# Optimization experiments

Hardware: AMD Instinct MI355X
Metric: run time of the kernel (lower is better)

## Reference

```python
import jax, jax.numpy as jnp
import numpy as np

H = 4096          # hidden_size
NH = 32           # num query heads
NKV = 8           # num kv heads
HD = H // NH      # head_dim = 128
NE = 8            # num_experts
TOPK = 2
ROPE_THETA = 10000.0
EPS = 1e-6


def rmsnorm(x, w):
    var = jnp.mean(x * x, axis=-1, keepdims=True)
    return x * jax.lax.rsqrt(var + EPS) * w


def apply_rope_neox(x, positions):
    # x: [N, heads, HD]; neox style: rotate halves
    half = HD // 2
    inv_freq = 1.0 / (ROPE_THETA ** (jnp.arange(0, HD, 2, dtype=jnp.float32) / HD))  # [half]
    ang = positions.astype(jnp.float32)[:, None] * inv_freq[None, :]                 # [N, half]
    cos = jnp.cos(ang)[:, None, :]  # [N,1,half]
    sin = jnp.sin(ang)[:, None, :]
    x1, x2 = x[..., :half], x[..., half:]
    return jnp.concatenate([x1 * cos - x2 * sin, x2 * cos + x1 * sin], axis=-1)


def setup_inputs() -> dict:
    key = jax.random.key(0)
    ks = jax.random.split(key, 6)
    N = 2048
    return {
        "positions": jnp.arange(N, dtype=jnp.int32),
        "hidden_states": jax.random.normal(ks[0], (N, H), dtype=jnp.float32),
        "w_qkv": jax.random.normal(ks[1], (H, (NH + 2 * NKV) * HD), dtype=jnp.float32) * 0.02,
        "w_o": jax.random.normal(ks[2], (NH * HD, H), dtype=jnp.float32) * 0.02,
        "w_gate": jax.random.normal(ks[3], (H, NE), dtype=jnp.float32) * 0.02,
        "rms_w_pre": jnp.ones((H,), dtype=jnp.float32),
        "rms_w_post": jnp.ones((H,), dtype=jnp.float32),
        "expert_logits": jax.random.uniform(ks[4], (N, NE), dtype=jnp.float32),
    }


def reference(positions, hidden_states, w_qkv, w_o, w_gate, rms_w_pre, rms_w_post, expert_logits):
    N = hidden_states.shape[0]
    # pre-attention RMSNorm (residual is None branch)
    residual = hidden_states
    x = rmsnorm(hidden_states, rms_w_pre)

    qkv = x @ w_qkv
    q = qkv[:, : NH * HD].reshape(N, NH, HD)
    k = qkv[:, NH * HD : (NH + NKV) * HD].reshape(N, NKV, HD)
    v = qkv[:, (NH + NKV) * HD :].reshape(N, NKV, HD)

    q = apply_rope_neox(q, positions)
    k = apply_rope_neox(k, positions)

    # GQA causal self-attention (prefill, single sequence)
    group = NH // NKV
    k_rep = jnp.repeat(k, group, axis=1)  # [N, NH, HD]
    v_rep = jnp.repeat(v, group, axis=1)
    scale = HD ** -0.5
    scores = jnp.einsum("qhd,khd->hqk", q, k_rep) * scale  # [NH, N, N]
    causal = jnp.tril(jnp.ones((N, N), dtype=bool))
    scores = jnp.where(causal[None], scores, jnp.finfo(scores.dtype).min)
    probs = jax.nn.softmax(scores, axis=-1)
    attn_out = jnp.einsum("hqk,khd->qhd", probs, v_rep).reshape(N, NH * HD)

    output = attn_out @ w_o
    # post-attention RMSNorm with fused residual add (vLLM semantics)
    s = output + residual
    residual = s
    output = rmsnorm(s, rms_w_post)

    router_logits = output @ w_gate  # computed as in source; routing result overwritten below

    # random_routing: topk over random expert logits, renormalized
    topk_weights, topk_ids = jax.lax.top_k(expert_logits, TOPK)  # [N, TOPK]
    topk_weights = topk_weights / jnp.sum(topk_weights, axis=-1, keepdims=True)

    # permute_by_exp_ids: stable sort of flattened expert ids, gather tokens
    reorder_ids = jnp.argsort(topk_ids.reshape(-1), stable=True)  # [N*TOPK]
    permuted_output = output[reorder_ids // TOPK]                 # [N*TOPK, H]
    return permuted_output, topk_weights, topk_ids, reorder_ids
```

## Files before the change

kernel.cpp:

```cpp
#include <hip/hip_runtime.h>
#include <hip/hip_bf16.h>
#include <math.h>

#define N_TOK 2048
#define H_DIM 4096
#define NH 32
#define NKV 8
#define HD 128
#define QKV_D 6144
#define NE 8
#define TOPK 2

#define OUT_PERM 0
#define OUT_W    16777216
#define OUT_IDS  16781312
#define OUT_REO  16785408

typedef __bf16 bf16x8 __attribute__((ext_vector_type(8)));
typedef float f32x4 __attribute__((ext_vector_type(4)));

typedef __attribute__((address_space(3))) void lds_void;
typedef __attribute__((address_space(1))) const void gbl_void;

__device__ __forceinline__ void gld16(const void* g, void* l) {
    __builtin_amdgcn_global_load_lds((gbl_void*)g, (lds_void*)l, 16, 0, 0);
}

__device__ __forceinline__ unsigned short f2bf(float f) {
    union { float f; unsigned u; } v; v.f = f;
    unsigned r = v.u + 0x7fff + ((v.u >> 16) & 1);
    return (unsigned short)(r >> 16);
}
__device__ __forceinline__ unsigned pack2bf(float a, float b) {
    return (unsigned)f2bf(a) | ((unsigned)f2bf(b) << 16);
}
__device__ __forceinline__ float bf2f(unsigned short u) {
    union { unsigned u; float f; } v; v.u = ((unsigned)u) << 16;
    return v.f;
}

__global__ __launch_bounds__(256) void rmsnorm_k(const float* __restrict__ x,
                                                 const float* __restrict__ w,
                                                 float* __restrict__ yf,
                                                 unsigned short* __restrict__ yb) {
    int row = blockIdx.x;
    int tid = threadIdx.x;
    const float4* x4 = (const float4*)(x + (size_t)row * H_DIM);
    const float4* w4 = (const float4*)w;
    float4 v[4];
    float ss = 0.f;
#pragma unroll
    for (int k = 0; k < 4; ++k) {
        v[k] = x4[tid + k * 256];
        ss += v[k].x * v[k].x + v[k].y * v[k].y + v[k].z * v[k].z + v[k].w * v[k].w;
    }
#pragma unroll
    for (int off = 32; off; off >>= 1) ss += __shfl_xor(ss, off);
    __shared__ float sacc[4];
    if ((tid & 63) == 0) sacc[tid >> 6] = ss;
    __syncthreads();
    float tot = sacc[0] + sacc[1] + sacc[2] + sacc[3];
    float sc = rsqrtf(tot * (1.0f / H_DIM) + 1e-6f);
#pragma unroll
    for (int k = 0; k < 4; ++k) {
        float4 ww = w4[tid + k * 256];
        float4 o;
        o.x = v[k].x * sc * ww.x;
        o.y = v[k].y * sc * ww.y;
        o.z = v[k].z * sc * ww.z;
        o.w = v[k].w * sc * ww.w;
        if (yf) {
            *(float4*)(yf + (size_t)row * H_DIM + (tid + k * 256) * 4) = o;
        } else {
            uint2 p;
            p.x = pack2bf(o.x, o.y);
            p.y = pack2bf(o.z, o.w);
            *(uint2*)(yb + (size_t)row * H_DIM + (tid + k * 256) * 4) = p;
        }
    }
}

__global__ __launch_bounds__(256) void convT_k(const float* __restrict__ src,
                                               unsigned short* __restrict__ dst,
                                               int R, int C) {
    __shared__ float t[64][68];
    int r0 = blockIdx.y * 64, c0 = blockIdx.x * 64;
    int tid = threadIdx.x;
    int lr = tid >> 4, lc = tid & 15;
#pragma unroll
    for (int it = 0; it < 4; ++it) {
        int r = lr + it * 16;
        float4 v = *(const float4*)(src + (size_t)(r0 + r) * C + c0 + lc * 4);
        *(float4*)&t[r][lc * 4] = v;
    }
    __syncthreads();
#pragma unroll
    for (int it = 0; it < 4; ++it) {
        int cc = lr + it * 16;
        uint2 o;
        o.x = pack2bf(t[lc * 4 + 0][cc], t[lc * 4 + 1][cc]);
        o.y = pack2bf(t[lc * 4 + 2][cc], t[lc * 4 + 3][cc]);
        *(uint2*)(dst + (size_t)(c0 + cc) * R + r0 + lc * 4) = o;
    }
}

__global__ __launch_bounds__(256) void gemm_k(const __hip_bfloat16* __restrict__ A,
                                              const __hip_bfloat16* __restrict__ Bt,
                                              float* __restrict__ C,
                                              unsigned short* __restrict__ Cb,
                                              const float* __restrict__ residual,
                                              int Ncols) {
    __shared__ __align__(16) __hip_bfloat16 As[128 * 64];
    __shared__ __align__(16) __hip_bfloat16 Bs[128 * 64];
    const int K = H_DIM;
    int tid = threadIdx.x, w = tid >> 6, lane = tid & 63;
    int quad = lane >> 4, l15 = lane & 15;
    int m0 = blockIdx.x * 128, n0 = blockIdx.y * 128;
    int wm = (w & 1) * 64, wn = (w >> 1) * 64;

    int rowInChunk = lane >> 3;
    int uIdx = lane & 7;
    const char* Ag[4]; const char* Bg[4];
    char* Al[4]; char* Bl[4];
#pragma unroll
    for (int c = 0; c < 4; ++c) {
        int ch = w * 4 + c;
        int r = ch * 8 + rowInChunk;
        int gu = uIdx ^ (r & 7);
        Ag[c] = (const char*)(A + (size_t)(m0 + r) * K) + gu * 16;
        Bg[c] = (const char*)(Bt + (size_t)(n0 + r) * K) + gu * 16;
        Al[c] = (char*)As + ch * 1024;
        Bl[c] = (char*)Bs + ch * 1024;
    }

    f32x4 acc[4][4];
#pragma unroll
    for (int i = 0; i < 4; ++i)
#pragma unroll
        for (int j = 0; j < 4; ++j) acc[i][j] = (f32x4){0.f, 0.f, 0.f, 0.f};

    for (int k0 = 0; k0 < K; k0 += 64) {
        __syncthreads();
#pragma unroll
        for (int c = 0; c < 4; ++c) gld16(Ag[c] + (size_t)k0 * 2, Al[c]);
#pragma unroll
        for (int c = 0; c < 4; ++c) gld16(Bg[c] + (size_t)k0 * 2, Bl[c]);
        __syncthreads();
#pragma unroll
        for (int kk = 0; kk < 2; ++kk) {
            bf16x8 af[4], bfr[4];
#pragma unroll
            for (int mt = 0; mt < 4; ++mt) {
                int m = wm + mt * 16 + l15;
                af[mt] = *(const bf16x8*)((const char*)As + m * 128 + (((kk * 4 + quad) ^ (m & 7)) * 16));
            }
#pragma unroll
            for (int nt = 0; nt < 4; ++nt) {
                int n = wn + nt * 16 + l15;
                bfr[nt] = *(const bf16x8*)((const char*)Bs + n * 128 + (((kk * 4 + quad) ^ (n & 7)) * 16));
            }
#pragma unroll
            for (int mt = 0; mt < 4; ++mt)
#pragma unroll
                for (int nt = 0; nt < 4; ++nt)
                    acc[mt][nt] = __builtin_amdgcn_mfma_f32_16x16x32_bf16(af[mt], bfr[nt], acc[mt][nt], 0, 0, 0);
        }
    }
#pragma unroll
    for (int mt = 0; mt < 4; ++mt)
#pragma unroll
        for (int nt = 0; nt < 4; ++nt)
#pragma unroll
            for (int r = 0; r < 4; ++r) {
                int row = m0 + wm + mt * 16 + quad * 4 + r;
                int col = n0 + wn + nt * 16 + l15;
                size_t off = (size_t)row * Ncols + col;
                float v = acc[mt][nt][r];
                if (Cb) {
                    Cb[off] = f2bf(v);
                } else {
                    if (residual) v += residual[off];
                    C[off] = v;
                }
            }
}

__global__ __launch_bounds__(256) void prep_k(const unsigned short* __restrict__ qkvb,
                                              const int* __restrict__ pos,
                                              unsigned short* __restrict__ Qc,
                                              unsigned short* __restrict__ Kc) {
    int row = blockIdx.x, tid = threadIdx.x;
    float fpos = (float)pos[row];
    const float scale = 0.08838834764831845f;
    const float lg = 0.20762050593045f;
#pragma unroll
    for (int it = 0; it < 8; ++it) {
        int pi = tid + it * 256;
        int head = pi >> 6, t = pi & 63;
        float inv = exp2f(-(float)t * lg);
        float ang = fpos * inv;
        float s = __sinf(ang), c = __cosf(ang);
        const unsigned short* bp = qkvb + (size_t)row * QKV_D + head * HD + t;
        float x1 = bf2f(bp[0]), x2 = bf2f(bp[64]);
        unsigned short* qb = Qc + (size_t)row * H_DIM + head * HD + t;
        qb[0]  = f2bf((x1 * c - x2 * s) * scale);
        qb[64] = f2bf((x2 * c + x1 * s) * scale);
    }
#pragma unroll
    for (int it = 0; it < 2; ++it) {
        int pi = tid + it * 256;
        int kvh = pi >> 6, t = pi & 63;
        float inv = exp2f(-(float)t * lg);
        float ang = fpos * inv;
        float s = __sinf(ang), c = __cosf(ang);
        const unsigned short* bp = qkvb + (size_t)row * QKV_D + H_DIM + kvh * HD + t;
        float x1 = bf2f(bp[0]), x2 = bf2f(bp[64]);
        unsigned short* kb = Kc + ((size_t)kvh * N_TOK + row) * HD + t;
        kb[0]  = f2bf(x1 * c - x2 * s);
        kb[64] = f2bf(x2 * c + x1 * s);
    }
}

__global__ __launch_bounds__(256) void vt_k(const unsigned short* __restrict__ qkvb,
                                            unsigned short* __restrict__ Vt) {
    __shared__ unsigned short ts[64][136];
    int j0 = blockIdx.x * 64, kvh = blockIdx.y, tid = threadIdx.x;
#pragma unroll
    for (int it = 0; it < 4; ++it) {
        int idx = tid + it * 256;
        int r = idx >> 4, c8 = idx & 15;
        *(uint4*)&ts[r][c8 * 8] =
            *(const uint4*)(qkvb + (size_t)(j0 + r) * QKV_D + (NH + NKV) * HD + kvh * HD + c8 * 8);
    }
    __syncthreads();
    int d = tid >> 1, half = tid & 1;
    unsigned short* dst = Vt + ((size_t)kvh * HD + d) * N_TOK + j0 + half * 32;
#pragma unroll
    for (int g = 0; g < 4; ++g) {
        int kb = half * 32 + g * 8;
        uint4 o;
        o.x = (unsigned)ts[kb + 0][d] | ((unsigned)ts[kb + 1][d] << 16);
        o.y = (unsigned)ts[kb + 2][d] | ((unsigned)ts[kb + 3][d] << 16);
        o.z = (unsigned)ts[kb + 4][d] | ((unsigned)ts[kb + 5][d] << 16);
        o.w = (unsigned)ts[kb + 6][d] | ((unsigned)ts[kb + 7][d] << 16);
        *(uint4*)(dst + g * 8) = o;
    }
}

__global__ __launch_bounds__(256) void attn_k(const __hip_bfloat16* __restrict__ Qc,
                                              const __hip_bfloat16* __restrict__ Kc,
                                              const __hip_bfloat16* __restrict__ Vt,
                                              unsigned short* __restrict__ ao) {
    __shared__ __align__(16) __hip_bfloat16 Ks[32 * 128];
    __shared__ __align__(16) __hip_bfloat16 Vs[128 * 32];
    __shared__ __align__(16) unsigned short Pw[4][16 * 40];

    int tid = threadIdx.x, w = tid >> 6, lane = tid & 63;
    int quad = lane >> 4, l15 = lane & 15;
    int h = blockIdx.y, kvh = h >> 2;
    int qt = gridDim.x - 1 - blockIdx.x;
    int i0 = qt * 64;
    int i0q = i0 + w * 16;
    int q = i0q + l15;

    bf16x8 qf[4];
    const __hip_bfloat16* qrow = Qc + (size_t)q * H_DIM + h * HD;
#pragma unroll
    for (int kf = 0; kf < 4; ++kf)
        qf[kf] = *(const bf16x8*)(qrow + kf * 32 + quad * 8);

    const char* KcH = (const char*)(Kc + (size_t)kvh * N_TOK * HD);
    const char* VtH = (const char*)(Vt + (size_t)kvh * HD * N_TOK);

    int chA = w * 2, chB = chA + 1;
    int kKeyA = chA * 4 + (lane >> 4), kKeyB = chB * 4 + (lane >> 4);
    int kPartA = (lane & 15) ^ (kKeyA & 15), kPartB = (lane & 15) ^ (kKeyB & 15);
    int vDA = chA * 16 + (lane >> 2), vDB = chB * 16 + (lane >> 2);
    int vPA = (lane & 3) ^ (vDA & 3), vPB = (lane & 3) ^ (vDB & 3);
    char* KlA = (char*)Ks + chA * 1024;
    char* KlB = (char*)Ks + chB * 1024;
    char* VlA = (char*)Vs + chA * 1024;
    char* VlB = (char*)Vs + chB * 1024;

    float mstat = -INFINITY, lstat = 0.f;
    f32x4 o[8];
#pragma unroll
    for (int nt = 0; nt < 8; ++nt) o[nt] = (f32x4){0.f, 0.f, 0.f, 0.f};

    for (int j0 = 0; j0 < i0 + 64; j0 += 32) {
        __syncthreads();
        gld16(KcH + (size_t)(j0 + kKeyA) * 256 + kPartA * 16, KlA);
        gld16(KcH + (size_t)(j0 + kKeyB) * 256 + kPartB * 16, KlB);
        gld16(VtH + (size_t)vDA * (N_TOK * 2) + (size_t)j0 * 2 + vPA * 16, VlA);
        gld16(VtH + (size_t)vDB * (N_TOK * 2) + (size_t)j0 * 2 + vPB * 16, VlB);
        __syncthreads();
        if (j0 > i0q + 15) continue;

        f32x4 s[2];
        s[0] = (f32x4){0.f, 0.f, 0.f, 0.f};
        s[1] = (f32x4){0.f, 0.f, 0.f, 0.f};
#pragma unroll
        for (int mt = 0; mt < 2; ++mt) {
            int key = mt * 16 + l15;
#pragma unroll
            for (int kf = 0; kf < 4; ++kf) {
                bf16x8 kfr = *(const bf16x8*)((const char*)Ks + key * 256 + (((kf * 4 + quad) ^ (key & 15)) * 16));
                s[mt] = __builtin_amdgcn_mfma_f32_16x16x32_bf16(kfr, qf[kf], s[mt], 0, 0, 0);
            }
        }
        if (j0 + 31 > i0q) {
#pragma unroll
            for (int mt = 0; mt < 2; ++mt) {
                int keyb = j0 + mt * 16 + quad * 4;
#pragma unroll
                for (int r = 0; r < 4; ++r)
                    if (keyb + r > q) s[mt][r] = -INFINITY;
            }
        }
        float mx = fmaxf(fmaxf(fmaxf(s[0][0], s[0][1]), fmaxf(s[0][2], s[0][3])),
                         fmaxf(fmaxf(s[1][0], s[1][1]), fmaxf(s[1][2], s[1][3])));
        mx = fmaxf(mx, __shfl_xor(mx, 16));
        mx = fmaxf(mx, __shfl_xor(mx, 32));
        float newm = fmaxf(mstat, mx);
        float alpha = __expf(mstat - newm);
        float p[8];
#pragma unroll
        for (int mt = 0; mt < 2; ++mt)
#pragma unroll
            for (int r = 0; r < 4; ++r) p[mt * 4 + r] = __expf(s[mt][r] - newm);
        float ps = p[0] + p[1] + p[2] + p[3] + p[4] + p[5] + p[6] + p[7];
        ps += __shfl_xor(ps, 16);
        ps += __shfl_xor(ps, 32);
        lstat = lstat * alpha + ps;
        mstat = newm;

        unsigned* pwb = (unsigned*)(&Pw[w][0]);
        int eo = l15 * 20 + quad * 2;
        pwb[eo]     = pack2bf(p[0], p[1]);
        pwb[eo + 1] = pack2bf(p[2], p[3]);
        pwb[eo + 8] = pack2bf(p[4], p[5]);
        pwb[eo + 9] = pack2bf(p[6], p[7]);
        bf16x8 pf = *(const bf16x8*)(&Pw[w][l15 * 40 + quad * 8]);

        float alq[4];
#pragma unroll
        for (int r = 0; r < 4; ++r) alq[r] = __shfl(alpha, quad * 4 + r);
#pragma unroll
        for (int nt = 0; nt < 8; ++nt)
#pragma unroll
            for (int r = 0; r < 4; ++r) o[nt][r] *= alq[r];

#pragma unroll
        for (int nt = 0; nt < 8; ++nt) {
            int d = nt * 16 + l15;
            bf16x8 vf = *(const bf16x8*)((const char*)Vs + d * 64 + ((quad ^ (d & 3)) * 16));
            o[nt] = __builtin_amdgcn_mfma_f32_16x16x32_bf16(pf, vf, o[nt], 0, 0, 0);
        }
    }

    float linv[4];
#pragma unroll
    for (int r = 0; r < 4; ++r) linv[r] = 1.f / __shfl(lstat, quad * 4 + r);
#pragma unroll
    for (int nt = 0; nt < 8; ++nt)
#pragma unroll
        for (int r = 0; r < 4; ++r) {
            int row = i0q + quad * 4 + r;
            int col = h * HD + nt * 16 + l15;
            ao[(size_t)row * H_DIM + col] = f2bf(o[nt][r] * linv[r]);
        }
}

__global__ __launch_bounds__(256) void topk_k(const float* __restrict__ elog,
                                              float* __restrict__ w_out,
                                              float* __restrict__ id_out,
                                              int* __restrict__ ids_int) {
    int row = blockIdx.x * 256 + threadIdx.x;
    if (row >= N_TOK) return;
    const float4* e4 = (const float4*)(elog + (size_t)row * NE);
    float4 a = e4[0], b = e4[1];
    float e[8] = {a.x, a.y, a.z, a.w, b.x, b.y, b.z, b.w};
    int id0 = 0;
    float b0 = e[0];
#pragma unroll
    for (int t = 1; t < 8; ++t)
        if (e[t] > b0) { b0 = e[t]; id0 = t; }
    int id1 = -1;
    float b1 = -INFINITY;
#pragma unroll
    for (int t = 0; t < 8; ++t)
        if (t != id0 && e[t] > b1) { b1 = e[t]; id1 = t; }
    float s = b0 + b1;
    w_out[row * 2 + 0] = b0 / s;
    w_out[row * 2 + 1] = b1 / s;
    id_out[row * 2 + 0] = (float)id0;
    id_out[row * 2 + 1] = (float)id1;
    ids_int[row * 2 + 0] = id0;
    ids_int[row * 2 + 1] = id1;
}

__global__ __launch_bounds__(256) void sort_k(const int* __restrict__ ids,
                                              float* __restrict__ reorder_out,
                                              int* __restrict__ perm) {
    __shared__ int sh[N_TOK * TOPK];
    int tid = threadIdx.x;
    for (int r = tid; r < N_TOK * TOPK; r += 256) sh[r] = ids[r];
    __syncthreads();
    int i = blockIdx.x * 256 + tid;
    int e = sh[i];
    int rank = 0;
    for (int j = 0; j < N_TOK * TOPK; ++j) {
        int ej = sh[j];
        rank += (ej < e) ? 1 : ((ej == e && j < i) ? 1 : 0);
    }
    reorder_out[rank] = (float)i;
    perm[rank] = i;
}

__global__ __launch_bounds__(256) void gather_k(const float* __restrict__ src,
                                                const int* __restrict__ perm,
                                                float* __restrict__ dst) {
    int r = blockIdx.x;
    int srow = perm[r] >> 1;
    const float4* s4 = (const float4*)(src + (size_t)srow * H_DIM);
    float4* d4 = (float4*)(dst + (size_t)r * H_DIM);
    int tid = threadIdx.x;
#pragma unroll
    for (int k = 0; k < 4; ++k) d4[tid + k * 256] = s4[tid + k * 256];
}

extern "C" void kernel_launch(void* const* d_in, const int* in_sizes, int n_in,
                              void* d_out, int out_size, void* d_ws, size_t ws_size,
                              hipStream_t stream) {
    const int*   positions = (const int*)d_in[0];
    const float* hidden    = (const float*)d_in[1];
    const float* w_qkv     = (const float*)d_in[2];
    const float* w_o       = (const float*)d_in[3];
    const float* rms_pre   = (const float*)d_in[5];
    const float* rms_post  = (const float*)d_in[6];
    const float* elog      = (const float*)d_in[7];
    float* out = (float*)d_out;

    char* ws = (char*)d_ws;
    unsigned short* wqkvT = (unsigned short*)(ws);
    unsigned short* woT   = (unsigned short*)(ws);
    float*          post  = (float*)(ws + 33554432ULL);
    unsigned short* xn    = (unsigned short*)(ws + 50331648ULL);
    unsigned short* aout  = (unsigned short*)(ws + 50331648ULL);
    unsigned short* qkvb  = (unsigned short*)(ws + 67108864ULL);
    float*          sbuf  = (float*)(ws + 67108864ULL);
    unsigned short* Qc    = (unsigned short*)(ws + 117440512ULL);
    unsigned short* Kc    = (unsigned short*)(ws + 134217728ULL);
    unsigned short* Vt    = (unsigned short*)(ws + 138412032ULL);
    int* ids_int  = (int*)(ws + 142606336ULL);
    int* perm_int = (int*)(ws + 142622720ULL);

    convT_k<<<dim3(QKV_D / 64, H_DIM / 64), 256, 0, stream>>>(w_qkv, wqkvT, H_DIM, QKV_D);
    rmsnorm_k<<<N_TOK, 256, 0, stream>>>(hidden, rms_pre, nullptr, xn);
    gemm_k<<<dim3(N_TOK / 128, QKV_D / 128), 256, 0, stream>>>(
        (const __hip_bfloat16*)xn, (const __hip_bfloat16*)wqkvT, nullptr, qkvb, nullptr, QKV_D);
    convT_k<<<dim3(H_DIM / 64, H_DIM / 64), 256, 0, stream>>>(w_o, woT, H_DIM, H_DIM);
    prep_k<<<N_TOK, 256, 0, stream>>>(qkvb, positions, Qc, Kc);
    vt_k<<<dim3(N_TOK / 64, NKV), 256, 0, stream>>>(qkvb, Vt);
    attn_k<<<dim3(N_TOK / 64, NH), 256, 0, stream>>>(
        (const __hip_bfloat16*)Qc, (const __hip_bfloat16*)Kc, (const __hip_bfloat16*)Vt, aout);
    gemm_k<<<dim3(N_TOK / 128, H_DIM / 128), 256, 0, stream>>>(
        (const __hip_bfloat16*)aout, (const __hip_bfloat16*)woT, sbuf, nullptr, hidden, H_DIM);
    rmsnorm_k<<<N_TOK, 256, 0, stream>>>(sbuf, rms_post, post, nullptr);
    topk_k<<<N_TOK / 256, 256, 0, stream>>>(elog, out + OUT_W, out + OUT_IDS, ids_int);
    sort_k<<<(N_TOK * TOPK) / 256, 256, 0, stream>>>(ids_int, out + OUT_REO, perm_int);
    gather_k<<<N_TOK * TOPK, 256, 0, stream>>>(post, perm_int, out + OUT_PERM);
}
```

Before: 799.9 us.

## Share KV tiles across two GQA heads per block and double-buffer K/V loads

The attention kernel now runs 512-thread blocks in which the 8 waves cover two query heads that share one KV head, so each K/V tile loaded into LDS serves twice as many heads. K/V tiles are double-buffered: the next tile is prefetched with async global-to-LDS loads while the current one is computed, which cuts the per-step barriers from two to one. The aim is to reduce K/V global traffic and hide load latency. The cost is doubled LDS for K/V, larger blocks that may lower occupancy, and half as many blocks in the grid.

```diff
diff --git a/kernel.cpp b/kernel.cpp
--- a/kernel.cpp
+++ b/kernel.cpp
@@ -247,20 +247,22 @@
     }
 }
 
-__global__ __launch_bounds__(256) void attn_k(const __hip_bfloat16* __restrict__ Qc,
+__global__ __launch_bounds__(512) void attn_k(const __hip_bfloat16* __restrict__ Qc,
                                               const __hip_bfloat16* __restrict__ Kc,
                                               const __hip_bfloat16* __restrict__ Vt,
                                               unsigned short* __restrict__ ao) {
-    __shared__ __align__(16) __hip_bfloat16 Ks[32 * 128];
-    __shared__ __align__(16) __hip_bfloat16 Vs[128 * 32];
-    __shared__ __align__(16) unsigned short Pw[4][16 * 40];
+    __shared__ __align__(16) __hip_bfloat16 Ks[2][32 * 128];
+    __shared__ __align__(16) __hip_bfloat16 Vs[2][128 * 32];
+    __shared__ __align__(16) unsigned short Pw[8][16 * 40];
 
     int tid = threadIdx.x, w = tid >> 6, lane = tid & 63;
     int quad = lane >> 4, l15 = lane & 15;
-    int h = blockIdx.y, kvh = h >> 2;
+    int pr = blockIdx.y;
+    int kvh = pr >> 1;
+    int h = kvh * 4 + (pr & 1) * 2 + (w & 1);
     int qt = gridDim.x - 1 - blockIdx.x;
     int i0 = qt * 64;
-    int i0q = i0 + w * 16;
+    int i0q = i0 + (w >> 1) * 16;
     int q = i0q + l15;
 
     bf16x8 qf[4];
@@ -272,90 +274,98 @@
     const char* KcH = (const char*)(Kc + (size_t)kvh * N_TOK * HD);
     const char* VtH = (const char*)(Vt + (size_t)kvh * HD * N_TOK);
 
-    int chA = w * 2, chB = chA + 1;
-    int kKeyA = chA * 4 + (lane >> 4), kKeyB = chB * 4 + (lane >> 4);
-    int kPartA = (lane & 15) ^ (kKeyA & 15), kPartB = (lane & 15) ^ (kKeyB & 15);
-    int vDA = chA * 16 + (lane >> 2), vDB = chB * 16 + (lane >> 2);
-    int vPA = (lane & 3) ^ (vDA & 3), vPB = (lane & 3) ^ (vDB & 3);
-    char* KlA = (char*)Ks + chA * 1024;
-    char* KlB = (char*)Ks + chB * 1024;
-    char* VlA = (char*)Vs + chA * 1024;
-    char* VlB = (char*)Vs + chB * 1024;
+    int kKey = w * 4 + (lane >> 4);
+    int kPart = (lane & 15) ^ (kKey & 15);
+    int vD = w * 16 + (lane >> 2);
+    int vP = (lane & 3) ^ (vD & 3);
+    char* Kl[2] = { (char*)&Ks[0][0] + w * 1024, (char*)&Ks[1][0] + w * 1024 };
+    char* Vl[2] = { (char*)&Vs[0][0] + w * 1024, (char*)&Vs[1][0] + w * 1024 };
 
     float mstat = -INFINITY, lstat = 0.f;
     f32x4 o[8];
 #pragma unroll
     for (int nt = 0; nt < 8; ++nt) o[nt] = (f32x4){0.f, 0.f, 0.f, 0.f};
 
-    for (int j0 = 0; j0 < i0 + 64; j0 += 32) {
+    int nsteps = (i0 + 64) >> 5;
+
+    gld16(KcH + (size_t)kKey * 256 + kPart * 16, Kl[0]);
+    gld16(VtH + (size_t)vD * (N_TOK * 2) + vP * 16, Vl[0]);
+    __syncthreads();
+
+    for (int t = 0; t < nsteps; ++t) {
+        int j0 = t << 5;
+        int cur = t & 1;
+        if (t + 1 < nsteps) {
+            int jn = j0 + 32;
+            gld16(KcH + (size_t)(jn + kKey) * 256 + kPart * 16, Kl[cur ^ 1]);
+            gld16(VtH + (size_t)vD * (N_TOK * 2) + (size_t)jn * 2 + vP * 16, Vl[cur ^ 1]);
+        }
+        if (j0 <= i0q + 15) {
+            const char* Kb = (const char*)&Ks[cur][0];
+            const char* Vb = (const char*)&Vs[cur][0];
+
+            f32x4 s[2];
+            s[0] = (f32x4){0.f, 0.f, 0.f, 0.f};
+            s[1] = (f32x4){0.f, 0.f, 0.f, 0.f};
+#pragma unroll
+            for (int mt = 0; mt < 2; ++mt) {
+                int key = mt * 16 + l15;
+#pragma unroll
+                for (int kf = 0; kf < 4; ++kf) {
+                    bf16x8 kfr = *(const bf16x8*)(Kb + key * 256 + (((kf * 4 + quad) ^ (key & 15)) * 16));
+                    s[mt] = __builtin_amdgcn_mfma_f32_16x16x32_bf16(kfr, qf[kf], s[mt], 0, 0, 0);
+                }
+            }
+            if (j0 + 31 > i0q) {
+#pragma unroll
+                for (int mt = 0; mt < 2; ++mt) {
+                    int keyb = j0 + mt * 16 + quad * 4;
+#pragma unroll
+                    for (int r = 0; r < 4; ++r)
+                        if (keyb + r > q) s[mt][r] = -INFINITY;
+                }
+            }
+            float mx = fmaxf(fmaxf(fmaxf(s[0][0], s[0][1]), fmaxf(s[0][2], s[0][3])),
+                             fmaxf(fmaxf(s[1][0], s[1][1]), fmaxf(s[1][2], s[1][3])));
+            mx = fmaxf(mx, __shfl_xor(mx, 16));
+            mx = fmaxf(mx, __shfl_xor(mx, 32));
+            float newm = fmaxf(mstat, mx);
+            float alpha = __expf(mstat - newm);
+            float p[8];
+#pragma unroll
+            for (int mt = 0; mt < 2; ++mt)
+#pragma unroll
+                for (int r = 0; r < 4; ++r) p[mt * 4 + r] = __expf(s[mt][r] - newm);
+            float ps = p[0] + p[1] + p[2] + p[3] + p[4] + p[5] + p[6] + p[7];
+            ps += __shfl_xor(ps, 16);
+            ps += __shfl_xor(ps, 32);
+            lstat = lstat * alpha + ps;
+            mstat = newm;
+
+            unsigned* pwb = (unsigned*)(&Pw[w][0]);
+            int eo = l15 * 20 + quad * 2;
+            pwb[eo]     = pack2bf(p[0], p[1]);
+            pwb[eo + 1] = pack2bf(p[2], p[3]);
+            pwb[eo + 8] = pack2bf(p[4], p[5]);
+            pwb[eo + 9] = pack2bf(p[6], p[7]);
+            bf16x8 pf = *(const bf16x8*)(&Pw[w][l15 * 40 + quad * 8]);
+
+            float alq[4];
+#pragma unroll
+            for (int r = 0; r < 4; ++r) alq[r] = __shfl(alpha, quad * 4 + r);
+#pragma unroll
+            for (int nt = 0; nt < 8; ++nt)
+#pragma unroll
+                for (int r = 0; r < 4; ++r) o[nt][r] *= alq[r];
+
+#pragma unroll
+            for (int nt = 0; nt < 8; ++nt) {
+                int d = nt * 16 + l15;
+                bf16x8 vf = *(const bf16x8*)(Vb + d * 64 + ((quad ^ (d & 3)) * 16));
+                o[nt] = __builtin_amdgcn_mfma_f32_16x16x32_bf16(pf, vf, o[nt], 0, 0, 0);
+            }
+        }
         __syncthreads();
-        gld16(KcH + (size_t)(j0 + kKeyA) * 256 + kPartA * 16, KlA);
-        gld16(KcH + (size_t)(j0 + kKeyB) * 256 + kPartB * 16, KlB);
-        gld16(VtH + (size_t)vDA * (N_TOK * 2) + (size_t)j0 * 2 + vPA * 16, VlA);
-        gld16(VtH + (size_t)vDB * (N_TOK * 2) + (size_t)j0 * 2 + vPB * 16, VlB);
-        __syncthreads();
-        if (j0 > i0q + 15) continue;
-
-        f32x4 s[2];
-        s[0] = (f32x4){0.f, 0.f, 0.f, 0.f};
-        s[1] = (f32x4){0.f, 0.f, 0.f, 0.f};
-#pragma unroll
-        for (int mt = 0; mt < 2; ++mt) {
-            int key = mt * 16 + l15;
-#pragma unroll
-            for (int kf = 0; kf < 4; ++kf) {
-                bf16x8 kfr = *(const bf16x8*)((const char*)Ks + key * 256 + (((kf * 4 + quad) ^ (key & 15)) * 16));
-                s[mt] = __builtin_amdgcn_mfma_f32_16x16x32_bf16(kfr, qf[kf], s[mt], 0, 0, 0);
-            }
-        }
-        if (j0 + 31 > i0q) {
-#pragma unroll
-            for (int mt = 0; mt < 2; ++mt) {
-                int keyb = j0 + mt * 16 + quad * 4;
-#pragma unroll
-                for (int r = 0; r < 4; ++r)
-                    if (keyb + r > q) s[mt][r] = -INFINITY;
-            }
-        }
-        float mx = fmaxf(fmaxf(fmaxf(s[0][0], s[0][1]), fmaxf(s[0][2], s[0][3])),
-                         fmaxf(fmaxf(s[1][0], s[1][1]), fmaxf(s[1][2], s[1][3])));
-        mx = fmaxf(mx, __shfl_xor(mx, 16));
-        mx = fmaxf(mx, __shfl_xor(mx, 32));
-        float newm = fmaxf(mstat, mx);
-        float alpha = __expf(mstat - newm);
-        float p[8];
-#pragma unroll
-        for (int mt = 0; mt < 2; ++mt)
-#pragma unroll
-            for (int r = 0; r < 4; ++r) p[mt * 4 + r] = __expf(s[mt][r] - newm);
-        float ps = p[0] + p[1] + p[2] + p[3] + p[4] + p[5] + p[6] + p[7];
-        ps += __shfl_xor(ps, 16);
-        ps += __shfl_xor(ps, 32);
-        lstat = lstat * alpha + ps;
-        mstat = newm;
-
-        unsigned* pwb = (unsigned*)(&Pw[w][0]);
-        int eo = l15 * 20 + quad * 2;
-        pwb[eo]     = pack2bf(p[0], p[1]);
-        pwb[eo + 1] = pack2bf(p[2], p[3]);
-        pwb[eo + 8] = pack2bf(p[4], p[5]);
-        pwb[eo + 9] = pack2bf(p[6], p[7]);
-        bf16x8 pf = *(const bf16x8*)(&Pw[w][l15 * 40 + quad * 8]);
-
-        float alq[4];
-#pragma unroll
-        for (int r = 0; r < 4; ++r) alq[r] = __shfl(alpha, quad * 4 + r);
-#pragma unroll
-        for (int nt = 0; nt < 8; ++nt)
-#pragma unroll
-            for (int r = 0; r < 4; ++r) o[nt][r] *= alq[r];
-
-#pragma unroll
-        for (int nt = 0; nt < 8; ++nt) {
-            int d = nt * 16 + l15;
-            bf16x8 vf = *(const bf16x8*)((const char*)Vs + d * 64 + ((quad ^ (d & 3)) * 16));
-            o[nt] = __builtin_amdgcn_mfma_f32_16x16x32_bf16(pf, vf, o[nt], 0, 0, 0);
-        }
     }
 
     float linv[4];
@@ -462,7 +472,7 @@
     convT_k<<<dim3(H_DIM / 64, H_DIM / 64), 256, 0, stream>>>(w_o, woT, H_DIM, H_DIM);
     prep_k<<<N_TOK, 256, 0, stream>>>(qkvb, positions, Qc, Kc);
     vt_k<<<dim3(N_TOK / 64, NKV), 256, 0, stream>>>(qkvb, Vt);
-    attn_k<<<dim3(N_TOK / 64, NH), 256, 0, stream>>>(
+    attn_k<<<dim3(N_TOK / 64, 16), 512, 0, stream>>>(
         (const __hip_bfloat16*)Qc, (const __hip_bfloat16*)Kc, (const __hip_bfloat16*)Vt, aout);
     gemm_k<<<dim3(N_TOK / 128, H_DIM / 128), 256, 0, stream>>>(
         (const __hip_bfloat16*)aout, (const __hip_bfloat16*)woT, sbuf, nullptr, hidden, H_DIM);
```

Result: faster. 768.2 us (-4.0%).
